# Kernel optimization log

Hardware: AMD Instinct MI355X
Metric: run time of the kernel (lower is better)

## Reference

```python
import jax, jax.numpy as jnp
import numpy as np


def setup_inputs() -> dict:
    key = jax.random.key(0)
    kx, km = jax.random.split(key)
    B, D, O = 16384, 256, 32
    x = jax.random.normal(kx, (B, D), dtype=jnp.float32)
    M = jax.random.uniform(km, (D, O), dtype=jnp.float32)
    return {"x": x, "M": M}


def reference(x, M):
    # NMU forward: y[b, o] = prod_d (M_hat[d, o] * x[b, d] + 1 - M_hat[d, o])
    M_hat = jnp.clip(M, 0.0, 1.0)                      # [D, O]
    # affine broadcast: [B, D, 1] * [1, D, O] -> [B, D, O]
    t = x[:, :, None] * M_hat[None, :, :] + (1.0 - M_hat)[None, :, :]
    return jnp.prod(t, axis=1)                          # [B, O]
```

## Files before the change

kernel.cpp:

```cpp
#include <hip/hip_runtime.h>


constexpr int D  = 256;
constexpr int O  = 32;
constexpr int SLOTS = 8;
constexpr int R  = 4;
constexpr int ROWS_PER_BLOCK = SLOTS * R;
constexpr int DC = 32;

__global__ __launch_bounds__(256) void nmu_fwd_kernel(
    const float* __restrict__ x, const float* __restrict__ M,
    float* __restrict__ y)
{
    const int o    = threadIdx.x & 31;
    const int slot = threadIdx.x >> 5;
    const int row0 = blockIdx.x * ROWS_PER_BLOCK + slot;

    float prod[R];
#pragma unroll
    for (int i = 0; i < R; ++i) prod[i] = 1.0f;

#pragma unroll
    for (int dc = 0; dc < D; dc += DC) {
        float mh[DC], om[DC];
#pragma unroll
        for (int j = 0; j < DC; ++j) {
            float v = M[(dc + j) * O + o];
            v = __builtin_amdgcn_fmed3f(v, 0.0f, 1.0f);
            mh[j] = v;
            om[j] = 1.0f - v;
        }

#pragma unroll
        for (int i = 0; i < R; ++i) {
            const int row = row0 + i * SLOTS;
            const float4* xp = reinterpret_cast<const float4*>(x + row * D + dc);
            float p = prod[i];
#pragma unroll
            for (int q = 0; q < DC / 4; ++q) {
                float4 xv = xp[q];
                float t0 = fmaf(xv.x, mh[4*q+0], om[4*q+0]);
                float t1 = fmaf(xv.y, mh[4*q+1], om[4*q+1]);
                float t2 = fmaf(xv.z, mh[4*q+2], om[4*q+2]);
                float t3 = fmaf(xv.w, mh[4*q+3], om[4*q+3]);
                p = p * ((t0 * t1) * (t2 * t3));
            }
            prod[i] = p;
        }
    }

#pragma unroll
    for (int i = 0; i < R; ++i) {
        const int row = row0 + i * SLOTS;
        y[row * O + o] = prod[i];
    }
}

extern "C" void kernel_launch(void* const* d_in, const int* in_sizes, int n_in,
                              void* d_out, int out_size, void* d_ws, size_t ws_size,
                              hipStream_t stream) {
    const float* x = (const float*)d_in[0];
    const float* M = (const float*)d_in[1];
    float* y = (float*)d_out;
    const int B = in_sizes[0] / D;
    dim3 grid(B / ROWS_PER_BLOCK);
    nmu_fwd_kernel<<<grid, 256, 0, stream>>>(x, M, y);
}
```

Before: 80.52 us.

## Restructure NMU kernel: row-per-lane, scalar-loaded clamped M, packed math, LDS reduction

A small prep kernel clamps M into the workspace. The main kernel then gives each lane one row and each wave one D-segment, reads M through constant (scalar) loads, computes with packed 2-wide float FMAs using the form 1 + m*(x-1), and combines the per-segment partial products through shared memory. This is meant to cut the redundant per-lane M loads and the VALU work per element. In exchange it adds a second launch, an LDS reduction step with a barrier, a hardcoded batch size, and a slightly different rounding order.

```diff
diff --git a/kernel.cpp b/kernel.cpp
--- a/kernel.cpp
+++ b/kernel.cpp
@@ -1,59 +1,82 @@
 #include <hip/hip_runtime.h>
+#include <stdint.h>
 
 
-constexpr int D  = 256;
-constexpr int O  = 32;
-constexpr int SLOTS = 8;
-constexpr int R  = 4;
-constexpr int ROWS_PER_BLOCK = SLOTS * R;
-constexpr int DC = 32;
+typedef float v2f __attribute__((ext_vector_type(2)));
+typedef __attribute__((address_space(4))) const float kfloat;
 
-__global__ __launch_bounds__(256) void nmu_fwd_kernel(
-    const float* __restrict__ x, const float* __restrict__ M,
-    float* __restrict__ y)
-{
-    const int o    = threadIdx.x & 31;
-    const int slot = threadIdx.x >> 5;
-    const int row0 = blockIdx.x * ROWS_PER_BLOCK + slot;
+constexpr int D = 256;
+constexpr int O = 32;
+constexpr int ROWS = 64;
+constexpr int SEGS = 8;
+constexpr int SEG_D = D / SEGS;
+constexpr int LSTR = SEGS * O + 4;
+constexpr int NBLK = 16384 / ROWS;
 
-    float prod[R];
+__global__ __launch_bounds__(256) void nmu_prep(const float* __restrict__ M,
+                                                float* __restrict__ MH) {
+    const int i = blockIdx.x * 256 + threadIdx.x;
+    MH[i] = __builtin_amdgcn_fmed3f(M[i], 0.0f, 1.0f);
+}
+
+__global__ __launch_bounds__(512) void nmu_main(const float* __restrict__ x,
+                                                const float* __restrict__ MH,
+                                                float* __restrict__ y) {
+    __shared__ float part[ROWS * LSTR];
+    const int tid  = threadIdx.x;
+    const int lane = tid & 63;
+    const int w    = tid >> 6;
+    const int row0 = blockIdx.x * ROWS;
+
+    const int segbase = __builtin_amdgcn_readfirstlane(w * SEG_D * O);
+    kfloat* mc = (kfloat*)(uintptr_t)MH + segbase;
+
+    const float4* xp = reinterpret_cast<const float4*>(
+        x + (row0 + lane) * D + w * SEG_D);
+
+    v2f prod[O / 2];
 #pragma unroll
-    for (int i = 0; i < R; ++i) prod[i] = 1.0f;
+    for (int i = 0; i < O / 2; ++i) prod[i] = (v2f){1.0f, 1.0f};
 
+#pragma unroll 2
+    for (int q = 0; q < SEG_D / 4; ++q) {
+        const float4 xv = xp[q];
+        const float xs[4] = {xv.x, xv.y, xv.z, xv.w};
 #pragma unroll
-    for (int dc = 0; dc < D; dc += DC) {
-        float mh[DC], om[DC];
+        for (int j = 0; j < 4; ++j) {
+            const float xm1 = xs[j] - 1.0f;
+            const v2f xm1v = {xm1, xm1};
+            const int dbase = (q * 4 + j) * O;
 #pragma unroll
-        for (int j = 0; j < DC; ++j) {
-            float v = M[(dc + j) * O + o];
-            v = __builtin_amdgcn_fmed3f(v, 0.0f, 1.0f);
-            mh[j] = v;
-            om[j] = 1.0f - v;
-        }
-
-#pragma unroll
-        for (int i = 0; i < R; ++i) {
-            const int row = row0 + i * SLOTS;
-            const float4* xp = reinterpret_cast<const float4*>(x + row * D + dc);
-            float p = prod[i];
-#pragma unroll
-            for (int q = 0; q < DC / 4; ++q) {
-                float4 xv = xp[q];
-                float t0 = fmaf(xv.x, mh[4*q+0], om[4*q+0]);
-                float t1 = fmaf(xv.y, mh[4*q+1], om[4*q+1]);
-                float t2 = fmaf(xv.z, mh[4*q+2], om[4*q+2]);
-                float t3 = fmaf(xv.w, mh[4*q+3], om[4*q+3]);
-                p = p * ((t0 * t1) * (t2 * t3));
+            for (int op = 0; op < O / 2; ++op) {
+                v2f mh;
+                mh.x = mc[dbase + 2 * op];
+                mh.y = mc[dbase + 2 * op + 1];
+                v2f t = mh * xm1v + (v2f){1.0f, 1.0f};
+                prod[op] *= t;
             }
-            prod[i] = p;
         }
     }
 
+    float* pb = &part[lane * LSTR + w * O];
 #pragma unroll
-    for (int i = 0; i < R; ++i) {
-        const int row = row0 + i * SLOTS;
-        y[row * O + o] = prod[i];
+    for (int o4 = 0; o4 < 8; ++o4) {
+        float4 v = {prod[2 * o4].x, prod[2 * o4].y,
+                    prod[2 * o4 + 1].x, prod[2 * o4 + 1].y};
+        *reinterpret_cast<float4*>(pb + o4 * 4) = v;
     }
+    __syncthreads();
+
+    const int row = tid >> 3;
+    const int o4  = tid & 7;
+    const float* cb = &part[row * LSTR + o4 * 4];
+    float4 acc = *reinterpret_cast<const float4*>(cb);
+#pragma unroll
+    for (int s = 1; s < SEGS; ++s) {
+        float4 v = *reinterpret_cast<const float4*>(cb + s * O);
+        acc.x *= v.x; acc.y *= v.y; acc.z *= v.z; acc.w *= v.w;
+    }
+    *reinterpret_cast<float4*>(y + (row0 + row) * O + o4 * 4) = acc;
 }
 
 extern "C" void kernel_launch(void* const* d_in, const int* in_sizes, int n_in,
@@ -61,8 +84,9 @@
                               hipStream_t stream) {
     const float* x = (const float*)d_in[0];
     const float* M = (const float*)d_in[1];
-    float* y = (float*)d_out;
-    const int B = in_sizes[0] / D;
-    dim3 grid(B / ROWS_PER_BLOCK);
-    nmu_fwd_kernel<<<grid, 256, 0, stream>>>(x, M, y);
+    float* y  = (float*)d_out;
+    float* MH = (float*)d_ws;
+
+    nmu_prep<<<dim3(D * O / 256), 256, 0, stream>>>(M, MH);
+    nmu_main<<<dim3(NBLK), 512, 0, stream>>>(x, MH, y);
 }
```

Result: slower. 83.28 us (+3.4%).
